# Kernel optimization log

Measured on AMD Instinct MI355X. Metric: run time of the kernel, lower is better.

The kernel has to match this reference:

```python
import jax, jax.numpy as jnp
import numpy as np

E = 1024  # n_embd
L = 24    # n_layer
F = 4 * E # ffn hidden

def _ln(x, w, b):
    mu = jnp.mean(x)
    xm = x - mu
    var = jnp.mean(xm * xm)
    return xm * jax.lax.rsqrt(var + 1e-5) * w + b

def setup_inputs() -> dict:
    key = jax.random.key(0)
    ks = jax.random.split(key, 24)
    n = lambda k, s, sc=0.02: jax.random.normal(k, s, dtype=jnp.float32) * sc
    u = lambda k, s, lo, hi: jax.random.uniform(k, s, dtype=jnp.float32, minval=lo, maxval=hi)
    x = jax.random.normal(ks[0], (E,), dtype=jnp.float32)
    statea = jax.random.normal(ks[1], (L, E), dtype=jnp.float32)   # prev ln1 output
    stateb = n(ks[2], (L, E), 0.1)                                  # wkv numerator accum
    statec = u(ks[3], (L, E), 0.5, 1.5)                             # wkv denominator accum (>0)
    stated = jax.random.normal(ks[4], (L, E), dtype=jnp.float32)   # prev ln2 output
    state = jnp.stack([statea, stateb, statec, stated])
    return {
        "x": x,
        "state": state,
        "ln1w": 1.0 + n(ks[5], (L, E)),
        "ln1b": n(ks[6], (L, E)),
        "ln2w": 1.0 + n(ks[7], (L, E)),
        "ln2b": n(ks[8], (L, E)),
        "time_decay": u(ks[9], (L, E), 0.5, 0.99),   # module stores exp(raw) -> positive
        "time_first": u(ks[10], (L, E), 0.1, 1.0),   # module stores exp(raw) -> positive
        "key": n(ks[11], (L, 3, E, E)),              # stack([kk, vv, -rr]) per layer
        "outputv": n(ks[12], (L, E, E)),
        "mix_k": u(ks[13], (L, E), 0.0, 1.0),
        "mix_v": u(ks[14], (L, E), 0.0, 1.0),
        "mix_r": u(ks[15], (L, E), 0.0, 1.0),
        "mix_k_ffn": u(ks[16], (L, E), 0.0, 1.0),
        "mix_r_ffn": u(ks[17], (L, E), 0.0, 1.0),
        "key_ffn": n(ks[18], (L, F, E)),
        "receptance_ffn": n(ks[19], (L, E, E)),      # module stores -w; sign absorbed in init
        "value_ffn": n(ks[20], (L, E, F)),
    }

def reference(x, state, ln1w, ln1b, ln2w, ln2b, time_decay, time_first, key,
              outputv, mix_k, mix_v, mix_r, mix_k_ffn, mix_r_ffn,
              key_ffn, receptance_ffn, value_ffn):
    statea, stateb, statec, stated = state  # each [L, E]
    # forward pre-multiplies time-mix params by the per-layer OLD state (before the loop)
    kktk = mix_k * statea
    vvtv = mix_v * statea
    rrtr = mix_r * statea
    tmk = mix_k_ffn * stated
    tmr = mix_r_ffn * stated

    def step(cx, per):
        (l1w, l1b, l2w, l2b, td, tf, kw, ow, kk, vv, rr, tk, tr,
         kfw, rfw, vfw, sb, sc) = per
        # --- SA (time mixing / WKV state update) ---
        xn = _ln(cx, l1w, l1b)
        k = jnp.exp(kw[0] @ (xn + kk))
        v = kw[1] @ (xn + vv)
        r = jnp.exp(kw[2] @ (xn + rr)) + 1.0   # kw[2] = -rr weight
        wn = sb + tf * k * v
        d = sc * r + tf * k * r
        sx = cx + ow @ (wn / d)
        sb2 = sb * td + k * v
        sc2 = sc * td + k
        # --- FF (channel mixing) ---
        x2 = _ln(sx, l2w, l2b)
        kf = jnp.square(jax.nn.relu(kfw @ (x2 + tk)))
        rf = jnp.exp(rfw @ (x2 + tr))
        out = sx + (vfw @ kf) / (1.0 + rf)
        return out, (xn, sb2, sc2, x2)

    xs = (ln1w, ln1b, ln2w, ln2b, time_decay, time_first, key, outputv,
          kktk, vvtv, rrtr, tmk, tmr, key_ffn, receptance_ffn, value_ffn,
          stateb, statec)
    x_out, (sa, sb, sc, sd) = jax.lax.scan(step, x, xs)
    return x_out, jnp.stack([sa, sb, sc, sd])
```

## Files before the change

### kernel.cpp

```cpp
#include <hip/hip_runtime.h>

#define EDIM 1024
#define LNUM 24
#define FDIM 4096
#define NB 256
#define NT 512

__device__ __forceinline__ float wave_sum(float v) {
#pragma unroll
    for (int off = 32; off > 0; off >>= 1) v += __shfl_xor(v, off, 64);
    return v;
}

__device__ __forceinline__ float2 cload2(const float* p) {
    double d = __hip_atomic_load((const double*)p, __ATOMIC_RELAXED,
                                 __HIP_MEMORY_SCOPE_AGENT);
    float2 r;
    __builtin_memcpy(&r, &d, 8);
    return r;
}
__device__ __forceinline__ float cload1(const float* p) {
    return __hip_atomic_load(p, __ATOMIC_RELAXED, __HIP_MEMORY_SCOPE_AGENT);
}
__device__ __forceinline__ void cstore1(float* p, float v) {
    __hip_atomic_store(p, v, __ATOMIC_RELAXED, __HIP_MEMORY_SCOPE_AGENT);
}

#define FENCE()                                  \
    do {                                         \
        asm volatile("" ::: "memory");           \
        __builtin_amdgcn_sched_barrier(0);       \
    } while (0)

__device__ __forceinline__ void lbar() {
    asm volatile("s_waitcnt lgkmcnt(0)" ::: "memory");
    __builtin_amdgcn_sched_barrier(0);
    __builtin_amdgcn_s_barrier();
    asm volatile("" ::: "memory");
    __builtin_amdgcn_sched_barrier(0);
}

template <int P>
__device__ __forceinline__ void gbar(unsigned* grp, unsigned* flags, unsigned& bi) {
    asm volatile("s_waitcnt vmcnt(%0) lgkmcnt(0)" ::"i"(P) : "memory");
    __builtin_amdgcn_sched_barrier(0);
    __builtin_amdgcn_s_barrier();
    const unsigned bi1 = bi + 1u;
    if (threadIdx.x == 0) {
        const int g = blockIdx.x & 7;
        unsigned o = __hip_atomic_fetch_add(&grp[g << 4], 1u, __ATOMIC_RELAXED,
                                            __HIP_MEMORY_SCOPE_AGENT);
        if ((o & 31u) == 31u) {
            const unsigned tgt = 32u * bi1;
            int guard = 0;
            for (;;) {
                unsigned mn = 0xffffffffu;
#pragma unroll
                for (int i = 0; i < 8; ++i) {
                    unsigned v = __hip_atomic_load(&grp[i << 4], __ATOMIC_RELAXED,
                                                   __HIP_MEMORY_SCOPE_AGENT);
                    mn = (v < mn) ? v : mn;
                }
                if (mn >= tgt) break;
                __builtin_amdgcn_s_sleep(1);
                if (++guard > (1 << 20)) break;
            }
#pragma unroll 4
            for (int j = 0; j < 32; ++j)
                __hip_atomic_store(&flags[(g + 8 * j) << 4], bi1, __ATOMIC_RELAXED,
                                   __HIP_MEMORY_SCOPE_AGENT);
        } else {
            int guard = 0;
            while (__hip_atomic_load(&flags[blockIdx.x << 4], __ATOMIC_RELAXED,
                                     __HIP_MEMORY_SCOPE_AGENT) < bi1) {
                __builtin_amdgcn_s_sleep(1);
                if (++guard > (1 << 20)) break;
            }
        }
    }
    __builtin_amdgcn_s_barrier();
    asm volatile("" ::: "memory");
    __builtin_amdgcn_sched_barrier(0);
    ++bi;
}

__device__ __forceinline__ float dot16(const float4& p0, const float4& p1,
                                       const float4& p2, const float4& p3,
                                       const float4& a, const float4& b,
                                       const float4& c, const float4& d) {
    return p0.x * a.x + p0.y * a.y + p0.z * a.z + p0.w * a.w +
           p1.x * b.x + p1.y * b.y + p1.z * b.z + p1.w * b.w +
           p2.x * c.x + p2.y * c.y + p2.z * c.z + p2.w * c.w +
           p3.x * d.x + p3.y * d.y + p3.z * d.z + p3.w * d.w;
}

__device__ __forceinline__ float dot1024_pref(const float4& p0, const float4& p1,
                                              const float4& p2, const float4& p3,
                                              const float* op, int lane) {
    const float4* o = (const float4*)op;
    return wave_sum(dot16(p0, p1, p2, p3, o[lane], o[lane + 64], o[lane + 128],
                          o[lane + 192]));
}

__device__ __forceinline__ float dot512_pref(const float4& p0, const float4& p1,
                                             const float* op, int lane) {
    const float4* o = (const float4*)op;
    const float4 a = o[lane], b4 = o[lane + 64];
    return wave_sum(p0.x * a.x + p0.y * a.y + p0.z * a.z + p0.w * a.w +
                    p1.x * b4.x + p1.y * b4.y + p1.z * b4.z + p1.w * b4.w);
}

__global__ __launch_bounds__(NT, 2) void rwkv_persistent(
    const float* __restrict__ x_in, const float* __restrict__ state,
    const float* __restrict__ ln1w, const float* __restrict__ ln1b,
    const float* __restrict__ ln2w, const float* __restrict__ ln2b,
    const float* __restrict__ td, const float* __restrict__ tf,
    const float* __restrict__ key, const float* __restrict__ ow,
    const float* __restrict__ mixk, const float* __restrict__ mixv,
    const float* __restrict__ mixr, const float* __restrict__ mixkf,
    const float* __restrict__ mixrf, const float* __restrict__ kffn,
    const float* __restrict__ rffn, const float* __restrict__ vffn,
    float* __restrict__ out, float* __restrict__ ws, unsigned* __restrict__ grp,
    unsigned* __restrict__ flags) {
    __shared__ float smem[FDIM + 32];
    float* red = smem + FDIM;

    float* xbuf = ws;
    float* sxbuf = ws + 1024;
    float* kbuf = ws + 2048;
    float* vbuf = ws + 3072;
    float* rbuf = ws + 4096;
    float* kfbuf = ws + 5120;
    float* rdiv = ws + 9216;

    float* sa_out = out + EDIM;
    float* sb_out = sa_out + LNUM * EDIM;
    float* sc_out = sb_out + LNUM * EDIM;
    float* sd_out = sc_out + LNUM * EDIM;

    const int t = threadIdx.x;
    const int b = blockIdx.x;
    const int w = t >> 6;
    const int lane = t & 63;
    const int gw = (b << 3) + w;
    const int rrow = (b << 2) + (w >> 1);
    const int rh = w & 1;
    const int drow = (b << 2) + (w >> 2);
    const int dch = w & 3;
    unsigned bi = 0;

    float4 pA0, pA1, pA2, pA3, rA0, rA1;
    float4 pB0, pB1;
    float4 pC10, pC11, pC12, pC13, pC20, pC21, pC22, pC23, rC0, rC1;
    float4 pD0, pD1, pD2, pD3, pD4, pD5, pD6, pD7;

    {
        const float4* qA = (const float4*)(key + ((size_t)gw << 10));
        pA0 = qA[lane]; pA1 = qA[lane + 64]; pA2 = qA[lane + 128]; pA3 = qA[lane + 192];
        const float4* qR =
            (const float4*)(key + ((size_t)(2048 + rrow) << 10) + (rh << 9));
        rA0 = qR[lane]; rA1 = qR[lane + 64];
    }

    for (int l = 0; l < LNUM; ++l) {
        const float* cx = (l == 0) ? x_in : xbuf;
        const float* owl = ow + (size_t)l * EDIM * EDIM;
        const float* kfl = kffn + (size_t)l * FDIM * EDIM;
        const float* rfl = rffn + (size_t)l * EDIM * EDIM;
        const float* vfl = vffn + (size_t)l * EDIM * FDIM;
        const int le = l * EDIM;

        {
            const float2 xv = cload2(cx + 2 * t);
            float s = xv.x + xv.y, s2 = xv.x * xv.x + xv.y * xv.y;
#pragma unroll
            for (int off = 32; off > 0; off >>= 1) {
                s += __shfl_xor(s, off, 64);
                s2 += __shfl_xor(s2, off, 64);
            }
            if (lane == 0) { red[w] = s; red[8 + w] = s2; }
            lbar();
            float ts = 0.0f, ts2 = 0.0f;
#pragma unroll
            for (int i = 0; i < 8; ++i) { ts += red[i]; ts2 += red[8 + i]; }
            const float mu = ts * (1.0f / 1024.0f);
            const float inv = rsqrtf(ts2 * (1.0f / 1024.0f) - mu * mu + 1e-5f);
            const float2 wv = ((const float2*)(ln1w + le))[t];
            const float2 bv = ((const float2*)(ln1b + le))[t];
            const float2 xn = make_float2((xv.x - mu) * inv * wv.x + bv.x,
                                          (xv.y - mu) * inv * wv.y + bv.y);
            if (b == 0) ((float2*)(sa_out + le))[t] = xn;
            const float2 sav = ((const float2*)(state + le))[t];
            const float2 mk = ((const float2*)(mixk + le))[t];
            const float2 mv = ((const float2*)(mixv + le))[t];
            const float2 mr = ((const float2*)(mixr + le))[t];
            ((float2*)smem)[t] = make_float2(xn.x + mk.x * sav.x, xn.y + mk.y * sav.y);
            ((float2*)(smem + 1024))[t] =
                make_float2(xn.x + mv.x * sav.x, xn.y + mv.y * sav.y);
            ((float2*)(smem + 2048))[t] =
                make_float2(xn.x + mr.x * sav.x, xn.y + mr.y * sav.y);
            lbar();
            const int mat = gw >> 10;
            const float d1 = dot1024_pref(pA0, pA1, pA2, pA3, smem + (mat << 10), lane);
            if (lane == 0) {
                if (mat == 0) cstore1(kbuf + gw, expf(d1));
                else          cstore1(vbuf + gw - 1024, d1);
            }
            const float d2 = dot512_pref(rA0, rA1, smem + 2048 + (rh << 9), lane);
            if (lane == 0) red[16 + w] = d2;
            lbar();
            if (t < 4)
                cstore1(rbuf + (b << 2) + t,
                        expf(red[16 + 2 * t] + red[17 + 2 * t]) + 1.0f);
        }
        FENCE();
        {
            const float4* qB = (const float4*)(owl + ((size_t)rrow << 10) + (rh << 9));
            pB0 = qB[lane]; pB1 = qB[lane + 64];
            const float4* q1 = (const float4*)(kfl + ((size_t)gw << 10));
            pC10 = q1[lane]; pC11 = q1[lane + 64]; pC12 = q1[lane + 128]; pC13 = q1[lane + 192];
            const float4* q2 = (const float4*)(kfl + ((size_t)(gw + 2048) << 10));
            pC20 = q2[lane]; pC21 = q2[lane + 64]; pC22 = q2[lane + 128]; pC23 = q2[lane + 192];
            const float4* qR = (const float4*)(rfl + ((size_t)rrow << 10) + (rh << 9));
            rC0 = qR[lane]; rC1 = qR[lane + 64];
        }
        gbar<12>(grp, flags, bi);

        {
            const float2 k2 = cload2(kbuf + 2 * t);
            const float2 v2 = cload2(vbuf + 2 * t);
            const float2 r2 = cload2(rbuf + 2 * t);
            const float2 tf2 = ((const float2*)(tf + le))[t];
            const float2 sb2 = ((const float2*)(state + 1 * LNUM * EDIM + le))[t];
            const float2 sc2 = ((const float2*)(state + 2 * LNUM * EDIM + le))[t];
            const float g0 =
                (sb2.x + tf2.x * k2.x * v2.x) / (sc2.x * r2.x + tf2.x * k2.x * r2.x);
            const float g1 =
                (sb2.y + tf2.y * k2.y * v2.y) / (sc2.y * r2.y + tf2.y * k2.y * r2.y);
            ((float2*)smem)[t] = make_float2(g0, g1);
            if (b == 0) {
                const float2 td2 = ((const float2*)(td + le))[t];
                ((float2*)(sb_out + le))[t] =
                    make_float2(sb2.x * td2.x + k2.x * v2.x, sb2.y * td2.y + k2.y * v2.y);
                ((float2*)(sc_out + le))[t] =
                    make_float2(sc2.x * td2.x + k2.x, sc2.y * td2.y + k2.y);
            }
            lbar();
            const float pd = dot512_pref(pB0, pB1, smem + (rh << 9), lane);
            if (lane == 0) red[w] = pd;
            lbar();
            if (t < 4) {
                const int r = (b << 2) + t;
                cstore1(sxbuf + r, cload1(cx + r) + red[2 * t] + red[2 * t + 1]);
            }
        }
        FENCE();
        {
            const float4* q1 = (const float4*)(vfl + ((size_t)drow << 12) + (dch << 10));
            pD0 = q1[lane]; pD1 = q1[lane + 64]; pD2 = q1[lane + 128]; pD3 = q1[lane + 192];
            const float4* q2 =
                (const float4*)(vfl + ((size_t)(drow + 2) << 12) + (dch << 10));
            pD4 = q2[lane]; pD5 = q2[lane + 64]; pD6 = q2[lane + 128]; pD7 = q2[lane + 192];
        }
        gbar<8>(grp, flags, bi);

        {
            const float2 sxv = cload2(sxbuf + 2 * t);
            float s = sxv.x + sxv.y, s2 = sxv.x * sxv.x + sxv.y * sxv.y;
#pragma unroll
            for (int off = 32; off > 0; off >>= 1) {
                s += __shfl_xor(s, off, 64);
                s2 += __shfl_xor(s2, off, 64);
            }
            if (lane == 0) { red[w] = s; red[8 + w] = s2; }
            lbar();
            float ts = 0.0f, ts2 = 0.0f;
#pragma unroll
            for (int i = 0; i < 8; ++i) { ts += red[i]; ts2 += red[8 + i]; }
            const float mu = ts * (1.0f / 1024.0f);
            const float inv = rsqrtf(ts2 * (1.0f / 1024.0f) - mu * mu + 1e-5f);
            const float2 wv = ((const float2*)(ln2w + le))[t];
            const float2 bv = ((const float2*)(ln2b + le))[t];
            const float2 x2 = make_float2((sxv.x - mu) * inv * wv.x + bv.x,
                                          (sxv.y - mu) * inv * wv.y + bv.y);
            if (b == 0) ((float2*)(sd_out + le))[t] = x2;
            const float2 sdv = ((const float2*)(state + 3 * LNUM * EDIM + le))[t];
            const float2 mkf = ((const float2*)(mixkf + le))[t];
            const float2 mrf = ((const float2*)(mixrf + le))[t];
            ((float2*)smem)[t] = make_float2(x2.x + mkf.x * sdv.x, x2.y + mkf.y * sdv.y);
            ((float2*)(smem + 1024))[t] =
                make_float2(x2.x + mrf.x * sdv.x, x2.y + mrf.y * sdv.y);
            lbar();
            const float d1 = dot1024_pref(pC10, pC11, pC12, pC13, smem, lane);
            if (lane == 0) { const float rl = fmaxf(d1, 0.0f); cstore1(kfbuf + gw, rl * rl); }
            const float d2 = dot1024_pref(pC20, pC21, pC22, pC23, smem, lane);
            if (lane == 0) { const float rl = fmaxf(d2, 0.0f); cstore1(kfbuf + gw + 2048, rl * rl); }
            const float d3 = dot512_pref(rC0, rC1, smem + 1024 + (rh << 9), lane);
            if (lane == 0) red[16 + w] = d3;
            lbar();
            if (t < 4)
                cstore1(rdiv + (b << 2) + t,
                        1.0f / (1.0f + expf(red[16 + 2 * t] + red[17 + 2 * t])));
        }
        gbar<0>(grp, flags, bi);

        {
            const double* kfd = (const double*)kfbuf;
#pragma unroll
            for (int j = 0; j < 4; ++j)
                ((double*)smem)[t + j * 512] = __hip_atomic_load(
                    kfd + t + j * 512, __ATOMIC_RELAXED, __HIP_MEMORY_SCOPE_AGENT);
            lbar();
            const float pd0 = dot1024_pref(pD0, pD1, pD2, pD3, smem + (dch << 10), lane);
            const float pd1 = dot1024_pref(pD4, pD5, pD6, pD7, smem + (dch << 10), lane);
            if (lane == 0) { red[w] = pd0; red[8 + w] = pd1; }
            lbar();
            if (t < 4) {
                const int r = (b << 2) + t;
                const float dsum =
                    red[4 * t] + red[4 * t + 1] + red[4 * t + 2] + red[4 * t + 3];
                const float val = cload1(sxbuf + r) + dsum * cload1(rdiv + r);
                if (l == LNUM - 1) out[r] = val;
                else cstore1(xbuf + r, val);
            }
        }
        if (l < LNUM - 1) {
            FENCE();
            {
                const float* keyn = key + (size_t)(l + 1) * 3 * EDIM * EDIM;
                const float4* qA = (const float4*)(keyn + ((size_t)gw << 10));
                pA0 = qA[lane]; pA1 = qA[lane + 64]; pA2 = qA[lane + 128]; pA3 = qA[lane + 192];
                const float4* qR =
                    (const float4*)(keyn + ((size_t)(2048 + rrow) << 10) + (rh << 9));
                rA0 = qR[lane]; rA1 = qR[lane + 64];
            }
            gbar<6>(grp, flags, bi);
        }
    }
}

extern "C" void kernel_launch(void* const* d_in, const int* in_sizes, int n_in,
                              void* d_out, int out_size, void* d_ws, size_t ws_size,
                              hipStream_t stream) {
    const float* x_in = (const float*)d_in[0];
    const float* state = (const float*)d_in[1];
    const float* ln1w = (const float*)d_in[2];
    const float* ln1b = (const float*)d_in[3];
    const float* ln2w = (const float*)d_in[4];
    const float* ln2b = (const float*)d_in[5];
    const float* td = (const float*)d_in[6];
    const float* tf = (const float*)d_in[7];
    const float* key = (const float*)d_in[8];
    const float* ow = (const float*)d_in[9];
    const float* mixk = (const float*)d_in[10];
    const float* mixv = (const float*)d_in[11];
    const float* mixr = (const float*)d_in[12];
    const float* mixkf = (const float*)d_in[13];
    const float* mixrf = (const float*)d_in[14];
    const float* kffn = (const float*)d_in[15];
    const float* rffn = (const float*)d_in[16];
    const float* vffn = (const float*)d_in[17];

    float* out = (float*)d_out;
    float* ws = (float*)d_ws;

    unsigned* bar = (unsigned*)((char*)d_ws + 48 * 1024);
    unsigned* grp = bar;
    unsigned* flags = bar + 1024;

    hipMemsetAsync(bar, 0, 24 * 1024, stream);
    rwkv_persistent<<<NB, NT, 0, stream>>>(x_in, state, ln1w, ln1b, ln2w, ln2b, td, tf,
                                           key, ow, mixk, mixv, mixr, mixkf, mixrf,
                                           kffn, rffn, vffn, out, ws, grp, flags);
}
```

Measured before the change: 537.5 us.

## Defer cross-wave reductions to consumers and rebalance prefetch across grid barriers

Removes the intra-block LDS reduction and extra block barrier after each matvec by writing per-wave partial sums (two or four halves) to global buffers. Each consumer block then sums the partials and applies the exp/sigmoid itself, so every block redundantly recombines the 1024-element vectors. Weight prefetch for the FFN key and receptance matrices moves into the SA-output phase, which evens out register pressure across barriers. Also drops the sleep in the barrier spin loop and spreads state output writes across different blocks. The cost is more global loads per block, one extra grid barrier at the end, and a larger workspace.

```diff
diff --git a/kernel.cpp b/kernel.cpp
--- a/kernel.cpp
+++ b/kernel.cpp
@@ -19,11 +19,13 @@
     __builtin_memcpy(&r, &d, 8);
     return r;
 }
-__device__ __forceinline__ float cload1(const float* p) {
-    return __hip_atomic_load(p, __ATOMIC_RELAXED, __HIP_MEMORY_SCOPE_AGENT);
-}
 __device__ __forceinline__ void cstore1(float* p, float v) {
     __hip_atomic_store(p, v, __ATOMIC_RELAXED, __HIP_MEMORY_SCOPE_AGENT);
+}
+__device__ __forceinline__ void cstore2(float* p, float2 v) {
+    double d;
+    __builtin_memcpy(&d, &v, 8);
+    __hip_atomic_store((double*)p, d, __ATOMIC_RELAXED, __HIP_MEMORY_SCOPE_AGENT);
 }
 
 #define FENCE()                                  \
@@ -62,10 +64,9 @@
                     mn = (v < mn) ? v : mn;
                 }
                 if (mn >= tgt) break;
-                __builtin_amdgcn_s_sleep(1);
                 if (++guard > (1 << 20)) break;
             }
-#pragma unroll 4
+#pragma unroll 8
             for (int j = 0; j < 32; ++j)
                 __hip_atomic_store(&flags[(g + 8 * j) << 4], bi1, __ATOMIC_RELAXED,
                                    __HIP_MEMORY_SCOPE_AGENT);
@@ -125,13 +126,15 @@
     __shared__ float smem[FDIM + 32];
     float* red = smem + FDIM;
 
-    float* xbuf = ws;
+    float* xmat = ws;
     float* sxbuf = ws + 1024;
     float* kbuf = ws + 2048;
     float* vbuf = ws + 3072;
-    float* rbuf = ws + 4096;
-    float* kfbuf = ws + 5120;
-    float* rdiv = ws + 9216;
+    float* rkh = ws + 4096;
+    float* sxh = ws + 6144;
+    float* kfbuf = ws + 8192;
+    float* rdh = ws + 12288;
+    float* xpart = ws + 14336;
 
     float* sa_out = out + EDIM;
     float* sb_out = sa_out + LNUM * EDIM;
@@ -147,6 +150,7 @@
     const int rh = w & 1;
     const int drow = (b << 2) + (w >> 2);
     const int dch = w & 3;
+    const bool slicer = ((t >> 1) == b);
     unsigned bi = 0;
 
     float4 pA0, pA1, pA2, pA3, rA0, rA1;
@@ -163,15 +167,31 @@
     }
 
     for (int l = 0; l < LNUM; ++l) {
-        const float* cx = (l == 0) ? x_in : xbuf;
         const float* owl = ow + (size_t)l * EDIM * EDIM;
         const float* kfl = kffn + (size_t)l * FDIM * EDIM;
         const float* rfl = rffn + (size_t)l * EDIM * EDIM;
         const float* vfl = vffn + (size_t)l * EDIM * FDIM;
         const int le = l * EDIM;
-
-        {
-            const float2 xv = cload2(cx + 2 * t);
+        const int bsel = (l << 2) & 255;
+
+        {
+            float2 xv;
+            if (l == 0) {
+                xv = ((const float2*)x_in)[t];
+            } else {
+                const float2 sx2 = cload2(sxbuf + 2 * t);
+                const float2 xp0 = cload2(xpart + 2 * t);
+                const float2 xp1 = cload2(xpart + 1024 + 2 * t);
+                const float2 xp2 = cload2(xpart + 2048 + 2 * t);
+                const float2 xp3 = cload2(xpart + 3072 + 2 * t);
+                const float2 rd0 = cload2(rdh + 2 * t);
+                const float2 rd1 = cload2(rdh + 1024 + 2 * t);
+                const float gx = 1.0f / (1.0f + expf(rd0.x + rd1.x));
+                const float gy = 1.0f / (1.0f + expf(rd0.y + rd1.y));
+                xv.x = sx2.x + (xp0.x + xp1.x + xp2.x + xp3.x) * gx;
+                xv.y = sx2.y + (xp0.y + xp1.y + xp2.y + xp3.y) * gy;
+                if (slicer) cstore2(xmat + 2 * t, xv);
+            }
             float s = xv.x + xv.y, s2 = xv.x * xv.x + xv.y * xv.y;
 #pragma unroll
             for (int off = 32; off > 0; off >>= 1) {
@@ -189,7 +209,7 @@
             const float2 bv = ((const float2*)(ln1b + le))[t];
             const float2 xn = make_float2((xv.x - mu) * inv * wv.x + bv.x,
                                           (xv.y - mu) * inv * wv.y + bv.y);
-            if (b == 0) ((float2*)(sa_out + le))[t] = xn;
+            if (b == bsel) ((float2*)(sa_out + le))[t] = xn;
             const float2 sav = ((const float2*)(state + le))[t];
             const float2 mk = ((const float2*)(mixk + le))[t];
             const float2 mv = ((const float2*)(mixv + le))[t];
@@ -207,11 +227,7 @@
                 else          cstore1(vbuf + gw - 1024, d1);
             }
             const float d2 = dot512_pref(rA0, rA1, smem + 2048 + (rh << 9), lane);
-            if (lane == 0) red[16 + w] = d2;
-            lbar();
-            if (t < 4)
-                cstore1(rbuf + (b << 2) + t,
-                        expf(red[16 + 2 * t] + red[17 + 2 * t]) + 1.0f);
+            if (lane == 0) cstore1(rkh + (rh << 10) + rrow, d2);
         }
         FENCE();
         {
@@ -219,17 +235,16 @@
             pB0 = qB[lane]; pB1 = qB[lane + 64];
             const float4* q1 = (const float4*)(kfl + ((size_t)gw << 10));
             pC10 = q1[lane]; pC11 = q1[lane + 64]; pC12 = q1[lane + 128]; pC13 = q1[lane + 192];
-            const float4* q2 = (const float4*)(kfl + ((size_t)(gw + 2048) << 10));
-            pC20 = q2[lane]; pC21 = q2[lane + 64]; pC22 = q2[lane + 128]; pC23 = q2[lane + 192];
-            const float4* qR = (const float4*)(rfl + ((size_t)rrow << 10) + (rh << 9));
-            rC0 = qR[lane]; rC1 = qR[lane + 64];
-        }
-        gbar<12>(grp, flags, bi);
+        }
+        gbar<6>(grp, flags, bi);
 
         {
             const float2 k2 = cload2(kbuf + 2 * t);
             const float2 v2 = cload2(vbuf + 2 * t);
-            const float2 r2 = cload2(rbuf + 2 * t);
+            const float2 r0 = cload2(rkh + 2 * t);
+            const float2 r1 = cload2(rkh + 1024 + 2 * t);
+            const float2 r2 = make_float2(expf(r0.x + r1.x) + 1.0f,
+                                          expf(r0.y + r1.y) + 1.0f);
             const float2 tf2 = ((const float2*)(tf + le))[t];
             const float2 sb2 = ((const float2*)(state + 1 * LNUM * EDIM + le))[t];
             const float2 sc2 = ((const float2*)(state + 2 * LNUM * EDIM + le))[t];
@@ -238,7 +253,7 @@
             const float g1 =
                 (sb2.y + tf2.y * k2.y * v2.y) / (sc2.y * r2.y + tf2.y * k2.y * r2.y);
             ((float2*)smem)[t] = make_float2(g0, g1);
-            if (b == 0) {
+            if (b == bsel + 1) {
                 const float2 td2 = ((const float2*)(td + le))[t];
                 ((float2*)(sb_out + le))[t] =
                     make_float2(sb2.x * td2.x + k2.x * v2.x, sb2.y * td2.y + k2.y * v2.y);
@@ -247,25 +262,25 @@
             }
             lbar();
             const float pd = dot512_pref(pB0, pB1, smem + (rh << 9), lane);
-            if (lane == 0) red[w] = pd;
-            lbar();
-            if (t < 4) {
-                const int r = (b << 2) + t;
-                cstore1(sxbuf + r, cload1(cx + r) + red[2 * t] + red[2 * t + 1]);
-            }
+            if (lane == 0) cstore1(sxh + (rh << 10) + rrow, pd);
         }
         FENCE();
         {
-            const float4* q1 = (const float4*)(vfl + ((size_t)drow << 12) + (dch << 10));
-            pD0 = q1[lane]; pD1 = q1[lane + 64]; pD2 = q1[lane + 128]; pD3 = q1[lane + 192];
-            const float4* q2 =
-                (const float4*)(vfl + ((size_t)(drow + 2) << 12) + (dch << 10));
-            pD4 = q2[lane]; pD5 = q2[lane + 64]; pD6 = q2[lane + 128]; pD7 = q2[lane + 192];
-        }
-        gbar<8>(grp, flags, bi);
-
-        {
-            const float2 sxv = cload2(sxbuf + 2 * t);
+            const float4* q2 = (const float4*)(kfl + ((size_t)(gw + 2048) << 10));
+            pC20 = q2[lane]; pC21 = q2[lane + 64]; pC22 = q2[lane + 128]; pC23 = q2[lane + 192];
+            const float4* qR = (const float4*)(rfl + ((size_t)rrow << 10) + (rh << 9));
+            rC0 = qR[lane]; rC1 = qR[lane + 64];
+        }
+        gbar<6>(grp, flags, bi);
+
+        {
+            float2 xl;
+            if (l == 0) xl = ((const float2*)x_in)[t];
+            else        xl = cload2(xmat + 2 * t);
+            const float2 h0 = cload2(sxh + 2 * t);
+            const float2 h1 = cload2(sxh + 1024 + 2 * t);
+            const float2 sxv = make_float2(xl.x + h0.x + h1.x, xl.y + h0.y + h1.y);
+            if (slicer) cstore2(sxbuf + 2 * t, sxv);
             float s = sxv.x + sxv.y, s2 = sxv.x * sxv.x + sxv.y * sxv.y;
 #pragma unroll
             for (int off = 32; off > 0; off >>= 1) {
@@ -283,7 +298,7 @@
             const float2 bv = ((const float2*)(ln2b + le))[t];
             const float2 x2 = make_float2((sxv.x - mu) * inv * wv.x + bv.x,
                                           (sxv.y - mu) * inv * wv.y + bv.y);
-            if (b == 0) ((float2*)(sd_out + le))[t] = x2;
+            if (b == bsel + 2) ((float2*)(sd_out + le))[t] = x2;
             const float2 sdv = ((const float2*)(state + 3 * LNUM * EDIM + le))[t];
             const float2 mkf = ((const float2*)(mixkf + le))[t];
             const float2 mrf = ((const float2*)(mixrf + le))[t];
@@ -296,13 +311,17 @@
             const float d2 = dot1024_pref(pC20, pC21, pC22, pC23, smem, lane);
             if (lane == 0) { const float rl = fmaxf(d2, 0.0f); cstore1(kfbuf + gw + 2048, rl * rl); }
             const float d3 = dot512_pref(rC0, rC1, smem + 1024 + (rh << 9), lane);
-            if (lane == 0) red[16 + w] = d3;
-            lbar();
-            if (t < 4)
-                cstore1(rdiv + (b << 2) + t,
-                        1.0f / (1.0f + expf(red[16 + 2 * t] + red[17 + 2 * t])));
-        }
-        gbar<0>(grp, flags, bi);
+            if (lane == 0) cstore1(rdh + (rh << 10) + rrow, d3);
+        }
+        FENCE();
+        {
+            const float4* q1 = (const float4*)(vfl + ((size_t)drow << 12) + (dch << 10));
+            pD0 = q1[lane]; pD1 = q1[lane + 64]; pD2 = q1[lane + 128]; pD3 = q1[lane + 192];
+            const float4* q2 =
+                (const float4*)(vfl + ((size_t)(drow + 2) << 12) + (dch << 10));
+            pD4 = q2[lane]; pD5 = q2[lane + 64]; pD6 = q2[lane + 128]; pD7 = q2[lane + 192];
+        }
+        gbar<8>(grp, flags, bi);
 
         {
             const double* kfd = (const double*)kfbuf;
@@ -313,15 +332,9 @@
             lbar();
             const float pd0 = dot1024_pref(pD0, pD1, pD2, pD3, smem + (dch << 10), lane);
             const float pd1 = dot1024_pref(pD4, pD5, pD6, pD7, smem + (dch << 10), lane);
-            if (lane == 0) { red[w] = pd0; red[8 + w] = pd1; }
-            lbar();
-            if (t < 4) {
-                const int r = (b << 2) + t;
-                const float dsum =
-                    red[4 * t] + red[4 * t + 1] + red[4 * t + 2] + red[4 * t + 3];
-                const float val = cload1(sxbuf + r) + dsum * cload1(rdiv + r);
-                if (l == LNUM - 1) out[r] = val;
-                else cstore1(xbuf + r, val);
+            if (lane == 0) {
+                cstore1(xpart + (dch << 10) + drow, pd0);
+                cstore1(xpart + (dch << 10) + drow + 2, pd1);
             }
         }
         if (l < LNUM - 1) {
@@ -336,6 +349,22 @@
             }
             gbar<6>(grp, flags, bi);
         }
+    }
+
+    FENCE();
+    gbar<0>(grp, flags, bi);
+    if (slicer) {
+        const float2 sx2 = cload2(sxbuf + 2 * t);
+        const float2 xp0 = cload2(xpart + 2 * t);
+        const float2 xp1 = cload2(xpart + 1024 + 2 * t);
+        const float2 xp2 = cload2(xpart + 2048 + 2 * t);
+        const float2 xp3 = cload2(xpart + 3072 + 2 * t);
+        const float2 rd0 = cload2(rdh + 2 * t);
+        const float2 rd1 = cload2(rdh + 1024 + 2 * t);
+        const float gx = 1.0f / (1.0f + expf(rd0.x + rd1.x));
+        const float gy = 1.0f / (1.0f + expf(rd0.y + rd1.y));
+        out[2 * t] = sx2.x + (xp0.x + xp1.x + xp2.x + xp3.x) * gx;
+        out[2 * t + 1] = sx2.y + (xp0.y + xp1.y + xp2.y + xp3.y) * gy;
     }
 }
 
@@ -364,7 +393,7 @@
     float* out = (float*)d_out;
     float* ws = (float*)d_ws;
 
-    unsigned* bar = (unsigned*)((char*)d_ws + 48 * 1024);
+    unsigned* bar = (unsigned*)((char*)d_ws + 96 * 1024);
     unsigned* grp = bar;
     unsigned* flags = bar + 1024;
 
```

New measurement: 520.0 us. -3.3%, faster.

## Compute layernorm per-wave from registers and simplify grid barrier release

Applied to the files above, without the earlier changes.

Each wave now loads the full activation vector and computes layernorm statistics with a single wave reduction instead of staging through shared memory with extra block barriers. The mixed inputs are formed on the fly in registers and dotted directly with the prefetched weights. The grid barrier releases waiters through 8 per-group flags instead of 256 per-block flags, and the leader stops sleeping while it spins. The result is fewer block barriers and less shared-memory traffic per layer, at the cost of redundant global loads per wave and more spinning on contended flags.

```diff
diff --git a/kernel.cpp b/kernel.cpp
--- a/kernel.cpp
+++ b/kernel.cpp
@@ -10,6 +10,14 @@
 #pragma unroll
     for (int off = 32; off > 0; off >>= 1) v += __shfl_xor(v, off, 64);
     return v;
+}
+__device__ __forceinline__ float2 wave_sum2(float a, float b) {
+#pragma unroll
+    for (int off = 32; off > 0; off >>= 1) {
+        a += __shfl_xor(a, off, 64);
+        b += __shfl_xor(b, off, 64);
+    }
+    return make_float2(a, b);
 }
 
 __device__ __forceinline__ float2 cload2(const float* p) {
@@ -19,6 +27,10 @@
     __builtin_memcpy(&r, &d, 8);
     return r;
 }
+__device__ __forceinline__ float4 cload4(const float* p) {
+    const float2 a = cload2(p), b = cload2(p + 2);
+    return make_float4(a.x, a.y, b.x, b.y);
+}
 __device__ __forceinline__ float cload1(const float* p) {
     return __hip_atomic_load(p, __ATOMIC_RELAXED, __HIP_MEMORY_SCOPE_AGENT);
 }
@@ -26,10 +38,10 @@
     __hip_atomic_store(p, v, __ATOMIC_RELAXED, __HIP_MEMORY_SCOPE_AGENT);
 }
 
-#define FENCE()                                  \
-    do {                                         \
-        asm volatile("" ::: "memory");           \
-        __builtin_amdgcn_sched_barrier(0);       \
+#define FENCE()                            \
+    do {                                   \
+        asm volatile("" ::: "memory");     \
+        __builtin_amdgcn_sched_barrier(0); \
     } while (0)
 
 __device__ __forceinline__ void lbar() {
@@ -41,15 +53,15 @@
 }
 
 template <int P>
-__device__ __forceinline__ void gbar(unsigned* grp, unsigned* flags, unsigned& bi) {
+__device__ __forceinline__ void gbar(unsigned* grp, unsigned* rel, unsigned& bi) {
     asm volatile("s_waitcnt vmcnt(%0) lgkmcnt(0)" ::"i"(P) : "memory");
     __builtin_amdgcn_sched_barrier(0);
     __builtin_amdgcn_s_barrier();
     const unsigned bi1 = bi + 1u;
     if (threadIdx.x == 0) {
         const int g = blockIdx.x & 7;
-        unsigned o = __hip_atomic_fetch_add(&grp[g << 4], 1u, __ATOMIC_RELAXED,
-                                            __HIP_MEMORY_SCOPE_AGENT);
+        const unsigned o = __hip_atomic_fetch_add(&grp[g << 4], 1u, __ATOMIC_RELAXED,
+                                                  __HIP_MEMORY_SCOPE_AGENT);
         if ((o & 31u) == 31u) {
             const unsigned tgt = 32u * bi1;
             int guard = 0;
@@ -57,24 +69,21 @@
                 unsigned mn = 0xffffffffu;
 #pragma unroll
                 for (int i = 0; i < 8; ++i) {
-                    unsigned v = __hip_atomic_load(&grp[i << 4], __ATOMIC_RELAXED,
-                                                   __HIP_MEMORY_SCOPE_AGENT);
-                    mn = (v < mn) ? v : mn;
+                    const unsigned v = __hip_atomic_load(
+                        &grp[i << 4], __ATOMIC_RELAXED, __HIP_MEMORY_SCOPE_AGENT);
+                    mn = v < mn ? v : mn;
                 }
                 if (mn >= tgt) break;
-                __builtin_amdgcn_s_sleep(1);
                 if (++guard > (1 << 20)) break;
             }
-#pragma unroll 4
-            for (int j = 0; j < 32; ++j)
-                __hip_atomic_store(&flags[(g + 8 * j) << 4], bi1, __ATOMIC_RELAXED,
-                                   __HIP_MEMORY_SCOPE_AGENT);
+            __hip_atomic_store(&rel[g << 4], bi1, __ATOMIC_RELAXED,
+                               __HIP_MEMORY_SCOPE_AGENT);
         } else {
             int guard = 0;
-            while (__hip_atomic_load(&flags[blockIdx.x << 4], __ATOMIC_RELAXED,
+            while (__hip_atomic_load(&rel[(blockIdx.x & 7) << 4], __ATOMIC_RELAXED,
                                      __HIP_MEMORY_SCOPE_AGENT) < bi1) {
                 __builtin_amdgcn_s_sleep(1);
-                if (++guard > (1 << 20)) break;
+                if (++guard > (1 << 22)) break;
             }
         }
     }
@@ -84,31 +93,54 @@
     ++bi;
 }
 
-__device__ __forceinline__ float dot16(const float4& p0, const float4& p1,
-                                       const float4& p2, const float4& p3,
-                                       const float4& a, const float4& b,
-                                       const float4& c, const float4& d) {
-    return p0.x * a.x + p0.y * a.y + p0.z * a.z + p0.w * a.w +
-           p1.x * b.x + p1.y * b.y + p1.z * b.z + p1.w * b.w +
-           p2.x * c.x + p2.y * c.y + p2.z * c.z + p2.w * c.w +
-           p3.x * d.x + p3.y * d.y + p3.z * d.z + p3.w * d.w;
-}
-
-__device__ __forceinline__ float dot1024_pref(const float4& p0, const float4& p1,
-                                              const float4& p2, const float4& p3,
-                                              const float* op, int lane) {
-    const float4* o = (const float4*)op;
-    return wave_sum(dot16(p0, p1, p2, p3, o[lane], o[lane + 64], o[lane + 128],
-                          o[lane + 192]));
-}
-
-__device__ __forceinline__ float dot512_pref(const float4& p0, const float4& p1,
-                                             const float* op, int lane) {
-    const float4* o = (const float4*)op;
-    const float4 a = o[lane], b4 = o[lane + 64];
-    return wave_sum(p0.x * a.x + p0.y * a.y + p0.z * a.z + p0.w * a.w +
-                    p1.x * b4.x + p1.y * b4.y + p1.z * b4.z + p1.w * b4.w);
-}
+__device__ __forceinline__ float dotp4(const float4& a, const float4& b) {
+    return a.x * b.x + a.y * b.y + a.z * b.z + a.w * b.w;
+}
+
+#define PHASE_A_Q(XQ, PA, QI)                                              \
+    {                                                                      \
+        const float4 lw = LW1[lane + QI * 64];                             \
+        const float4 lb = LB1[lane + QI * 64];                             \
+        const float4 av = SAv[lane + QI * 64];                             \
+        const float4 mx = MXv[lane + QI * 64];                             \
+        float4 xn, op;                                                     \
+        xn.x = (XQ.x - mu) * inv * lw.x + lb.x;                            \
+        xn.y = (XQ.y - mu) * inv * lw.y + lb.y;                            \
+        xn.z = (XQ.z - mu) * inv * lw.z + lb.z;                            \
+        xn.w = (XQ.w - mu) * inv * lw.w + lb.w;                            \
+        op.x = xn.x + mx.x * av.x; op.y = xn.y + mx.y * av.y;              \
+        op.z = xn.z + mx.z * av.z; op.w = xn.w + mx.w * av.w;              \
+        acc += dotp4(PA, op);                                              \
+        if ((QI >> 1) == rh) {                                             \
+            const float4 mr4 = MRv[lane + QI * 64];                        \
+            op.x = xn.x + mr4.x * av.x; op.y = xn.y + mr4.y * av.y;        \
+            op.z = xn.z + mr4.z * av.z; op.w = xn.w + mr4.w * av.w;        \
+            accR += dotp4(((QI & 1) ? rA1 : rA0), op);                     \
+        }                                                                  \
+    }
+
+#define PHASE_C_Q(SQ, PC1, PC2, QI)                                        \
+    {                                                                      \
+        const float4 lw = LW2[lane + QI * 64];                             \
+        const float4 lb = LB2[lane + QI * 64];                             \
+        const float4 sd4 = SDv[lane + QI * 64];                            \
+        const float4 mf = MKFv[lane + QI * 64];                            \
+        float4 x2, op;                                                     \
+        x2.x = (SQ.x - mu) * inv * lw.x + lb.x;                            \
+        x2.y = (SQ.y - mu) * inv * lw.y + lb.y;                            \
+        x2.z = (SQ.z - mu) * inv * lw.z + lb.z;                            \
+        x2.w = (SQ.w - mu) * inv * lw.w + lb.w;                            \
+        op.x = x2.x + mf.x * sd4.x; op.y = x2.y + mf.y * sd4.y;            \
+        op.z = x2.z + mf.z * sd4.z; op.w = x2.w + mf.w * sd4.w;            \
+        accF1 += dotp4(PC1, op);                                           \
+        accF2 += dotp4(PC2, op);                                           \
+        if ((QI >> 1) == rh) {                                             \
+            const float4 mr4 = MRFv[lane + QI * 64];                       \
+            op.x = x2.x + mr4.x * sd4.x; op.y = x2.y + mr4.y * sd4.y;      \
+            op.z = x2.z + mr4.z * sd4.z; op.w = x2.w + mr4.w * sd4.w;      \
+            accRF += dotp4(((QI & 1) ? rC1 : rC0), op);                    \
+        }                                                                  \
+    }
 
 __global__ __launch_bounds__(NT, 2) void rwkv_persistent(
     const float* __restrict__ x_in, const float* __restrict__ state,
@@ -121,32 +153,36 @@
     const float* __restrict__ mixrf, const float* __restrict__ kffn,
     const float* __restrict__ rffn, const float* __restrict__ vffn,
     float* __restrict__ out, float* __restrict__ ws, unsigned* __restrict__ grp,
-    unsigned* __restrict__ flags) {
-    __shared__ float smem[FDIM + 32];
-    float* red = smem + FDIM;
-
-    float* xbuf = ws;
-    float* sxbuf = ws + 1024;
-    float* kbuf = ws + 2048;
-    float* vbuf = ws + 3072;
-    float* rbuf = ws + 4096;
-    float* kfbuf = ws + 5120;
-    float* rdiv = ws + 9216;
+    unsigned* __restrict__ rel) {
+    __shared__ float red[32];
+
+    float* kbuf = ws;
+    float* vbuf = ws + 1024;
+    float* rbuf = ws + 2048;
+    float* sxbuf = ws + 3072;
+    float* kfbuf = ws + 4096;
+    float* xnext = ws + 8192;
 
     float* sa_out = out + EDIM;
     float* sb_out = sa_out + LNUM * EDIM;
     float* sc_out = sb_out + LNUM * EDIM;
     float* sd_out = sc_out + LNUM * EDIM;
+
+    const float* stB = state + 1 * LNUM * EDIM;
+    const float* stC = state + 2 * LNUM * EDIM;
 
     const int t = threadIdx.x;
     const int b = blockIdx.x;
     const int w = t >> 6;
     const int lane = t & 63;
     const int gw = (b << 3) + w;
+    const int mat = gw >> 10;
     const int rrow = (b << 2) + (w >> 1);
     const int rh = w & 1;
     const int drow = (b << 2) + (w >> 2);
     const int dch = w & 3;
+    const int eb = b << 2;
+    const int e0 = lane << 2;
     unsigned bi = 0;
 
     float4 pA0, pA1, pA2, pA3, rA0, rA1;
@@ -163,55 +199,69 @@
     }
 
     for (int l = 0; l < LNUM; ++l) {
-        const float* cx = (l == 0) ? x_in : xbuf;
         const float* owl = ow + (size_t)l * EDIM * EDIM;
         const float* kfl = kffn + (size_t)l * FDIM * EDIM;
         const float* rfl = rffn + (size_t)l * EDIM * EDIM;
         const float* vfl = vffn + (size_t)l * EDIM * FDIM;
         const int le = l * EDIM;
-
-        {
-            const float2 xv = cload2(cx + 2 * t);
-            float s = xv.x + xv.y, s2 = xv.x * xv.x + xv.y * xv.y;
-#pragma unroll
-            for (int off = 32; off > 0; off >>= 1) {
-                s += __shfl_xor(s, off, 64);
-                s2 += __shfl_xor(s2, off, 64);
-            }
-            if (lane == 0) { red[w] = s; red[8 + w] = s2; }
-            lbar();
-            float ts = 0.0f, ts2 = 0.0f;
-#pragma unroll
-            for (int i = 0; i < 8; ++i) { ts += red[i]; ts2 += red[8 + i]; }
-            const float mu = ts * (1.0f / 1024.0f);
-            const float inv = rsqrtf(ts2 * (1.0f / 1024.0f) - mu * mu + 1e-5f);
-            const float2 wv = ((const float2*)(ln1w + le))[t];
-            const float2 bv = ((const float2*)(ln1b + le))[t];
-            const float2 xn = make_float2((xv.x - mu) * inv * wv.x + bv.x,
-                                          (xv.y - mu) * inv * wv.y + bv.y);
-            if (b == 0) ((float2*)(sa_out + le))[t] = xn;
-            const float2 sav = ((const float2*)(state + le))[t];
-            const float2 mk = ((const float2*)(mixk + le))[t];
-            const float2 mv = ((const float2*)(mixv + le))[t];
-            const float2 mr = ((const float2*)(mixr + le))[t];
-            ((float2*)smem)[t] = make_float2(xn.x + mk.x * sav.x, xn.y + mk.y * sav.y);
-            ((float2*)(smem + 1024))[t] =
-                make_float2(xn.x + mv.x * sav.x, xn.y + mv.y * sav.y);
-            ((float2*)(smem + 2048))[t] =
-                make_float2(xn.x + mr.x * sav.x, xn.y + mr.y * sav.y);
-            lbar();
-            const int mat = gw >> 10;
-            const float d1 = dot1024_pref(pA0, pA1, pA2, pA3, smem + (mat << 10), lane);
+        float gt = 0.0f;
+
+        {
+            float4 xq0, xq1, xq2, xq3;
+            if (l == 0) {
+                const float4* xp = (const float4*)x_in;
+                xq0 = xp[lane]; xq1 = xp[lane + 64];
+                xq2 = xp[lane + 128]; xq3 = xp[lane + 192];
+            } else {
+                xq0 = cload4(xnext + e0);
+                xq1 = cload4(xnext + 256 + e0);
+                xq2 = cload4(xnext + 512 + e0);
+                xq3 = cload4(xnext + 768 + e0);
+            }
+            const float s = (xq0.x + xq0.y + xq0.z + xq0.w) +
+                            (xq1.x + xq1.y + xq1.z + xq1.w) +
+                            (xq2.x + xq2.y + xq2.z + xq2.w) +
+                            (xq3.x + xq3.y + xq3.z + xq3.w);
+            const float s2 = dotp4(xq0, xq0) + dotp4(xq1, xq1) +
+                             dotp4(xq2, xq2) + dotp4(xq3, xq3);
+            const float2 ss = wave_sum2(s, s2);
+            const float mu = ss.x * (1.0f / 1024.0f);
+            const float inv = rsqrtf(ss.y * (1.0f / 1024.0f) - mu * mu + 1e-5f);
+
+            const float4* LW1 = (const float4*)(ln1w + le);
+            const float4* LB1 = (const float4*)(ln1b + le);
+            const float4* SAv = (const float4*)(state + le);
+            const float4* MXv = (const float4*)((mat ? mixv : mixk) + le);
+            const float4* MRv = (const float4*)(mixr + le);
+            float acc = 0.0f, accR = 0.0f;
+            PHASE_A_Q(xq0, pA0, 0)
+            PHASE_A_Q(xq1, pA1, 1)
+            PHASE_A_Q(xq2, pA2, 2)
+            PHASE_A_Q(xq3, pA3, 3)
+            const float2 dv = wave_sum2(acc, accR);
             if (lane == 0) {
-                if (mat == 0) cstore1(kbuf + gw, expf(d1));
-                else          cstore1(vbuf + gw - 1024, d1);
-            }
-            const float d2 = dot512_pref(rA0, rA1, smem + 2048 + (rh << 9), lane);
-            if (lane == 0) red[16 + w] = d2;
+                if (mat == 0) cstore1(kbuf + gw, expf(dv.x));
+                else          cstore1(vbuf + gw - 1024, dv.x);
+                red[16 + w] = dv.y;
+            }
+            if (w == 0) {
+                const int q = b >> 6;
+                const float4 xs = q == 0 ? xq0 : q == 1 ? xq1 : q == 2 ? xq2 : xq3;
+                if (lane == (b & 63)) {
+                    const float4 lw = *(const float4*)(ln1w + le + eb);
+                    const float4 lb = *(const float4*)(ln1b + le + eb);
+                    float4 xn;
+                    xn.x = (xs.x - mu) * inv * lw.x + lb.x;
+                    xn.y = (xs.y - mu) * inv * lw.y + lb.y;
+                    xn.z = (xs.z - mu) * inv * lw.z + lb.z;
+                    xn.w = (xs.w - mu) * inv * lw.w + lb.w;
+                    *(float4*)(sa_out + le + eb) = xn;
+                    red[24] = xs.x; red[25] = xs.y; red[26] = xs.z; red[27] = xs.w;
+                }
+            }
             lbar();
             if (t < 4)
-                cstore1(rbuf + (b << 2) + t,
-                        expf(red[16 + 2 * t] + red[17 + 2 * t]) + 1.0f);
+                cstore1(rbuf + eb + t, expf(red[16 + 2 * t] + red[17 + 2 * t]) + 1.0f);
         }
         FENCE();
         {
@@ -219,40 +269,105 @@
             pB0 = qB[lane]; pB1 = qB[lane + 64];
             const float4* q1 = (const float4*)(kfl + ((size_t)gw << 10));
             pC10 = q1[lane]; pC11 = q1[lane + 64]; pC12 = q1[lane + 128]; pC13 = q1[lane + 192];
+        }
+        gbar<6>(grp, rel, bi);
+
+        {
+            float kj = 0.0f, vj = 0.0f;
+            if (t < 4) { kj = cload1(kbuf + eb + t); vj = cload1(vbuf + eb + t); }
+            const int gp0 = (rh << 9) + e0;
+            const int gp1 = gp0 + 256;
+            const float4 k0 = cload4(kbuf + gp0), k1 = cload4(kbuf + gp1);
+            const float4 v0 = cload4(vbuf + gp0), v1 = cload4(vbuf + gp1);
+            const float4 r0 = cload4(rbuf + gp0), r1 = cload4(rbuf + gp1);
+            const float4 tf0 = *(const float4*)(tf + le + gp0);
+            const float4 tf1 = *(const float4*)(tf + le + gp1);
+            const float4 sb0 = *(const float4*)(stB + le + gp0);
+            const float4 sb1 = *(const float4*)(stB + le + gp1);
+            const float4 sc0 = *(const float4*)(stC + le + gp0);
+            const float4 sc1 = *(const float4*)(stC + le + gp1);
+            float4 g0, g1;
+            g0.x = (sb0.x + tf0.x * k0.x * v0.x) / (sc0.x * r0.x + tf0.x * k0.x * r0.x);
+            g0.y = (sb0.y + tf0.y * k0.y * v0.y) / (sc0.y * r0.y + tf0.y * k0.y * r0.y);
+            g0.z = (sb0.z + tf0.z * k0.z * v0.z) / (sc0.z * r0.z + tf0.z * k0.z * r0.z);
+            g0.w = (sb0.w + tf0.w * k0.w * v0.w) / (sc0.w * r0.w + tf0.w * k0.w * r0.w);
+            g1.x = (sb1.x + tf1.x * k1.x * v1.x) / (sc1.x * r1.x + tf1.x * k1.x * r1.x);
+            g1.y = (sb1.y + tf1.y * k1.y * v1.y) / (sc1.y * r1.y + tf1.y * k1.y * r1.y);
+            g1.z = (sb1.z + tf1.z * k1.z * v1.z) / (sc1.z * r1.z + tf1.z * k1.z * r1.z);
+            g1.w = (sb1.w + tf1.w * k1.w * v1.w) / (sc1.w * r1.w + tf1.w * k1.w * r1.w);
+            const float pd = wave_sum(dotp4(pB0, g0) + dotp4(pB1, g1));
+            if (lane == 0) red[w] = pd;
+            if (t < 4) {
+                const int j = le + eb + t;
+                const float tdj = td[j];
+                sb_out[j] = stB[j] * tdj + kj * vj;
+                sc_out[j] = stC[j] * tdj + kj;
+            }
+            lbar();
+            if (t < 4)
+                cstore1(sxbuf + eb + t, red[24 + t] + red[2 * t] + red[2 * t + 1]);
+        }
+        FENCE();
+        {
             const float4* q2 = (const float4*)(kfl + ((size_t)(gw + 2048) << 10));
             pC20 = q2[lane]; pC21 = q2[lane + 64]; pC22 = q2[lane + 128]; pC23 = q2[lane + 192];
             const float4* qR = (const float4*)(rfl + ((size_t)rrow << 10) + (rh << 9));
             rC0 = qR[lane]; rC1 = qR[lane + 64];
         }
-        gbar<12>(grp, flags, bi);
-
-        {
-            const float2 k2 = cload2(kbuf + 2 * t);
-            const float2 v2 = cload2(vbuf + 2 * t);
-            const float2 r2 = cload2(rbuf + 2 * t);
-            const float2 tf2 = ((const float2*)(tf + le))[t];
-            const float2 sb2 = ((const float2*)(state + 1 * LNUM * EDIM + le))[t];
-            const float2 sc2 = ((const float2*)(state + 2 * LNUM * EDIM + le))[t];
-            const float g0 =
-                (sb2.x + tf2.x * k2.x * v2.x) / (sc2.x * r2.x + tf2.x * k2.x * r2.x);
-            const float g1 =
-                (sb2.y + tf2.y * k2.y * v2.y) / (sc2.y * r2.y + tf2.y * k2.y * r2.y);
-            ((float2*)smem)[t] = make_float2(g0, g1);
-            if (b == 0) {
-                const float2 td2 = ((const float2*)(td + le))[t];
-                ((float2*)(sb_out + le))[t] =
-                    make_float2(sb2.x * td2.x + k2.x * v2.x, sb2.y * td2.y + k2.y * v2.y);
-                ((float2*)(sc_out + le))[t] =
-                    make_float2(sc2.x * td2.x + k2.x, sc2.y * td2.y + k2.y);
+        gbar<6>(grp, rel, bi);
+
+        {
+            const float4 sq0 = cload4(sxbuf + e0);
+            const float4 sq1 = cload4(sxbuf + 256 + e0);
+            const float4 sq2 = cload4(sxbuf + 512 + e0);
+            const float4 sq3 = cload4(sxbuf + 768 + e0);
+            const float s = (sq0.x + sq0.y + sq0.z + sq0.w) +
+                            (sq1.x + sq1.y + sq1.z + sq1.w) +
+                            (sq2.x + sq2.y + sq2.z + sq2.w) +
+                            (sq3.x + sq3.y + sq3.z + sq3.w);
+            const float s2 = dotp4(sq0, sq0) + dotp4(sq1, sq1) +
+                             dotp4(sq2, sq2) + dotp4(sq3, sq3);
+            const float2 ss = wave_sum2(s, s2);
+            const float mu = ss.x * (1.0f / 1024.0f);
+            const float inv = rsqrtf(ss.y * (1.0f / 1024.0f) - mu * mu + 1e-5f);
+
+            const float4* LW2 = (const float4*)(ln2w + le);
+            const float4* LB2 = (const float4*)(ln2b + le);
+            const float4* SDv = (const float4*)(state + 3 * LNUM * EDIM + le);
+            const float4* MKFv = (const float4*)(mixkf + le);
+            const float4* MRFv = (const float4*)(mixrf + le);
+            float accF1 = 0.0f, accF2 = 0.0f, accRF = 0.0f;
+            PHASE_C_Q(sq0, pC10, pC20, 0)
+            PHASE_C_Q(sq1, pC11, pC21, 1)
+            PHASE_C_Q(sq2, pC12, pC22, 2)
+            PHASE_C_Q(sq3, pC13, pC23, 3)
+            const float2 df = wave_sum2(accF1, accF2);
+            const float dr = wave_sum(accRF);
+            if (lane == 0) {
+                float r1 = fmaxf(df.x, 0.0f);
+                float r2 = fmaxf(df.y, 0.0f);
+                cstore1(kfbuf + gw, r1 * r1);
+                cstore1(kfbuf + gw + 2048, r2 * r2);
+                red[16 + w] = dr;
+            }
+            if (w == 0) {
+                const int q = b >> 6;
+                const float4 xs = q == 0 ? sq0 : q == 1 ? sq1 : q == 2 ? sq2 : sq3;
+                if (lane == (b & 63)) {
+                    const float4 lw = *(const float4*)(ln2w + le + eb);
+                    const float4 lb = *(const float4*)(ln2b + le + eb);
+                    float4 x2;
+                    x2.x = (xs.x - mu) * inv * lw.x + lb.x;
+                    x2.y = (xs.y - mu) * inv * lw.y + lb.y;
+                    x2.z = (xs.z - mu) * inv * lw.z + lb.z;
+                    x2.w = (xs.w - mu) * inv * lw.w + lb.w;
+                    *(float4*)(sd_out + le + eb) = x2;
+                    red[28] = xs.x; red[29] = xs.y; red[30] = xs.z; red[31] = xs.w;
+                }
             }
             lbar();
-            const float pd = dot512_pref(pB0, pB1, smem + (rh << 9), lane);
-            if (lane == 0) red[w] = pd;
-            lbar();
-            if (t < 4) {
-                const int r = (b << 2) + t;
-                cstore1(sxbuf + r, cload1(cx + r) + red[2 * t] + red[2 * t + 1]);
-            }
+            if (t < 4)
+                gt = 1.0f / (1.0f + expf(red[16 + 2 * t] + red[17 + 2 * t]));
         }
         FENCE();
         {
@@ -262,66 +377,25 @@
                 (const float4*)(vfl + ((size_t)(drow + 2) << 12) + (dch << 10));
             pD4 = q2[lane]; pD5 = q2[lane + 64]; pD6 = q2[lane + 128]; pD7 = q2[lane + 192];
         }
-        gbar<8>(grp, flags, bi);
-
-        {
-            const float2 sxv = cload2(sxbuf + 2 * t);
-            float s = sxv.x + sxv.y, s2 = sxv.x * sxv.x + sxv.y * sxv.y;
-#pragma unroll
-            for (int off = 32; off > 0; off >>= 1) {
-                s += __shfl_xor(s, off, 64);
-                s2 += __shfl_xor(s2, off, 64);
-            }
-            if (lane == 0) { red[w] = s; red[8 + w] = s2; }
-            lbar();
-            float ts = 0.0f, ts2 = 0.0f;
-#pragma unroll
-            for (int i = 0; i < 8; ++i) { ts += red[i]; ts2 += red[8 + i]; }
-            const float mu = ts * (1.0f / 1024.0f);
-            const float inv = rsqrtf(ts2 * (1.0f / 1024.0f) - mu * mu + 1e-5f);
-            const float2 wv = ((const float2*)(ln2w + le))[t];
-            const float2 bv = ((const float2*)(ln2b + le))[t];
-            const float2 x2 = make_float2((sxv.x - mu) * inv * wv.x + bv.x,
-                                          (sxv.y - mu) * inv * wv.y + bv.y);
-            if (b == 0) ((float2*)(sd_out + le))[t] = x2;
-            const float2 sdv = ((const float2*)(state + 3 * LNUM * EDIM + le))[t];
-            const float2 mkf = ((const float2*)(mixkf + le))[t];
-            const float2 mrf = ((const float2*)(mixrf + le))[t];
-            ((float2*)smem)[t] = make_float2(x2.x + mkf.x * sdv.x, x2.y + mkf.y * sdv.y);
-            ((float2*)(smem + 1024))[t] =
-                make_float2(x2.x + mrf.x * sdv.x, x2.y + mrf.y * sdv.y);
-            lbar();
-            const float d1 = dot1024_pref(pC10, pC11, pC12, pC13, smem, lane);
-            if (lane == 0) { const float rl = fmaxf(d1, 0.0f); cstore1(kfbuf + gw, rl * rl); }
-            const float d2 = dot1024_pref(pC20, pC21, pC22, pC23, smem, lane);
-            if (lane == 0) { const float rl = fmaxf(d2, 0.0f); cstore1(kfbuf + gw + 2048, rl * rl); }
-            const float d3 = dot512_pref(rC0, rC1, smem + 1024 + (rh << 9), lane);
-            if (lane == 0) red[16 + w] = d3;
-            lbar();
-            if (t < 4)
-                cstore1(rdiv + (b << 2) + t,
-                        1.0f / (1.0f + expf(red[16 + 2 * t] + red[17 + 2 * t])));
-        }
-        gbar<0>(grp, flags, bi);
-
-        {
-            const double* kfd = (const double*)kfbuf;
-#pragma unroll
-            for (int j = 0; j < 4; ++j)
-                ((double*)smem)[t + j * 512] = __hip_atomic_load(
-                    kfd + t + j * 512, __ATOMIC_RELAXED, __HIP_MEMORY_SCOPE_AGENT);
-            lbar();
-            const float pd0 = dot1024_pref(pD0, pD1, pD2, pD3, smem + (dch << 10), lane);
-            const float pd1 = dot1024_pref(pD4, pD5, pD6, pD7, smem + (dch << 10), lane);
-            if (lane == 0) { red[w] = pd0; red[8 + w] = pd1; }
+        gbar<8>(grp, rel, bi);
+
+        {
+            const int kp = dch << 10;
+            const float4 o0 = cload4(kfbuf + kp + e0);
+            const float4 o1 = cload4(kfbuf + kp + 256 + e0);
+            const float4 o2 = cload4(kfbuf + kp + 512 + e0);
+            const float4 o3 = cload4(kfbuf + kp + 768 + e0);
+            const float2 dd = wave_sum2(
+                dotp4(pD0, o0) + dotp4(pD1, o1) + dotp4(pD2, o2) + dotp4(pD3, o3),
+                dotp4(pD4, o0) + dotp4(pD5, o1) + dotp4(pD6, o2) + dotp4(pD7, o3));
+            if (lane == 0) { red[w] = dd.x; red[8 + w] = dd.y; }
             lbar();
             if (t < 4) {
-                const int r = (b << 2) + t;
-                const float dsum =
+                const float ffn =
                     red[4 * t] + red[4 * t + 1] + red[4 * t + 2] + red[4 * t + 3];
-                const float val = cload1(sxbuf + r) + dsum * cload1(rdiv + r);
-                if (l == LNUM - 1) out[r] = val;
-                else cstore1(xbuf + r, val);
+                const float val = red[28 + t] + ffn * gt;
+                if (l == LNUM - 1) out[eb + t] = val;
+                else cstore1(xnext + eb + t, val);
             }
         }
         if (l < LNUM - 1) {
@@ -334,7 +408,7 @@
                     (const float4*)(keyn + ((size_t)(2048 + rrow) << 10) + (rh << 9));
                 rA0 = qR[lane]; rA1 = qR[lane + 64];
             }
-            gbar<6>(grp, flags, bi);
+            gbar<6>(grp, rel, bi);
         }
     }
 }
@@ -366,10 +440,10 @@
 
     unsigned* bar = (unsigned*)((char*)d_ws + 48 * 1024);
     unsigned* grp = bar;
-    unsigned* flags = bar + 1024;
-
-    hipMemsetAsync(bar, 0, 24 * 1024, stream);
+    unsigned* rel = bar + 256;
+
+    hipMemsetAsync(bar, 0, 2048, stream);
     rwkv_persistent<<<NB, NT, 0, stream>>>(x_in, state, ln1w, ln1b, ln2w, ln2b, td, tf,
                                            key, ow, mixk, mixv, mixr, mixkf, mixrf,
-                                           kffn, rffn, vffn, out, ws, grp, flags);
-}
+                                           kffn, rffn, vffn, out, ws, grp, rel);
+}
```

Measured after the change: 573.6 us, median of 2. +6.7%, slower.
